# Kernel optimization log

Hardware: AMD Instinct MI355X
Metric: run time of the kernel (lower is better)

Reference implementation:

```python
import jax, jax.numpy as jnp
import numpy as np

N = 50000   # drug nodes
R = 8       # relations (= n_classes)
E = 200000  # edges per relation
ED = 400000 # decoder edges


def _deg_norm(idx, n):
    deg = jax.ops.segment_sum(jnp.ones(idx.shape, jnp.float32), idx, num_segments=n)
    return jnp.where(deg > 0, jax.lax.rsqrt(jnp.maximum(deg, 1.0)), 0.0)


def hetero_conv(x, src, dst, W, b, n):
    # DGL HeteroGraphConv(sum) of GraphConv(norm='both') per relation, single node type.
    out = jnp.zeros((n, W.shape[2]), x.dtype)
    for r in range(W.shape[0]):
        s, d = src[r], dst[r]
        ns = _deg_norm(s, n)  # out-degree^{-1/2} (src norm)
        nd = _deg_norm(d, n)  # in-degree^{-1/2} (dst norm)
        m = (x * ns[:, None]) @ W[r]                       # [n, dout]
        agg = jax.ops.segment_sum(m[s], d, num_segments=n)  # gather+scatter [E, dout]
        out = out + agg * nd[:, None] + b[r]
    return out


def hgcn_layer(x, src, dst, Wa, ba, Wb, bb, n):
    h = hetero_conv(x, src, dst, Wa, ba, n)
    h = jax.nn.relu(h)
    return hetero_conv(h, src, dst, Wb, bb, n)


def setup_inputs() -> dict:
    key = jax.random.key(0)
    ks = jax.random.split(key, 16)
    s = 0.02
    return {
        "node2_features": jax.random.normal(ks[0], (N, 256), jnp.float32),
        "mpnn_features": jax.random.normal(ks[1], (N, 300), jnp.float32),
        "src": jax.random.randint(ks[2], (R, E), 0, N, jnp.int32),
        "dst": jax.random.randint(ks[3], (R, E), 0, N, jnp.int32),
        "dec_src": jax.random.randint(ks[4], (ED,), 0, N, jnp.int32),
        "dec_dst": jax.random.randint(ks[5], (ED,), 0, N, jnp.int32),
        "W2a": jax.random.normal(ks[6], (R, 256, 256), jnp.float32) * s,
        "b2a": jnp.zeros((R, 256), jnp.float32),
        "W2b": jax.random.normal(ks[7], (R, 256, 128), jnp.float32) * s,
        "b2b": jnp.zeros((R, 128), jnp.float32),
        "W3a": jax.random.normal(ks[8], (R, 300, 256), jnp.float32) * s,
        "b3a": jnp.zeros((R, 256), jnp.float32),
        "W3b": jax.random.normal(ks[9], (R, 256, 128), jnp.float32) * s,
        "b3b": jnp.zeros((R, 128), jnp.float32),
        "Wp1": jax.random.normal(ks[10], (512, 256), jnp.float32) * s,
        "bp1": jnp.zeros((256,), jnp.float32),
        "Wp2": jax.random.normal(ks[11], (256, R), jnp.float32) * s,
        "bp2": jnp.zeros((R,), jnp.float32),
    }


def reference(node2_features, mpnn_features, src, dst, dec_src, dec_dst,
              W2a, b2a, W2b, b2b, W3a, b3a, W3b, b3b, Wp1, bp1, Wp2, bp2):
    h2 = hgcn_layer(node2_features, src, dst, W2a, b2a, W2b, b2b, N)  # [N, 128]
    h3 = hgcn_layer(mpnn_features, src, dst, W3a, b3a, W3b, b3b, N)   # [N, 128]
    feat = jnp.concatenate([h2, h3], axis=1)                            # [N, 256]
    # edge-wise gather-concat-MLP (note: original has NO relu between W1 and W2)
    x = jnp.concatenate([feat[dec_src], feat[dec_dst]], axis=1)          # [ED, 512]
    score = (x @ Wp1 + bp1) @ Wp2 + bp2                                  # [ED, R]
    return score
```

## Files before the change

kernel.cpp:

```cpp
#include <hip/hip_runtime.h>
#include <hip/hip_bf16.h>

#define NN 50000
#define RR 8
#define EE 200000
#define EDD 400000
#define SCB 196
#define CH 5000

typedef __attribute__((ext_vector_type(8))) short short8;
typedef __attribute__((ext_vector_type(4))) float floatx4;

static __device__ __forceinline__ unsigned short f2bf(float f) {
    union { float f; unsigned u; } v; v.f = f;
    unsigned r = v.u + 0x7fff + ((v.u >> 16) & 1);
    return (unsigned short)(r >> 16);
}
static __device__ __forceinline__ float bf2f(unsigned short h) {
    union { unsigned u; float f; } v; v.u = ((unsigned)h) << 16;
    return v.f;
}
static __device__ __forceinline__ void gload_lds16(const unsigned short* g, unsigned short* l) {
    __builtin_amdgcn_global_load_lds(
        (const __attribute__((address_space(1))) void*)g,
        (__attribute__((address_space(3))) void*)l,
        16, 0, 0);
}

__global__ void k_hist(const int* __restrict__ src, const int* __restrict__ dst,
                       int* __restrict__ outdeg, int* __restrict__ indeg) {
    int i = blockIdx.x * blockDim.x + threadIdx.x;
    if (i >= RR * EE) return;
    int r = i / EE;
    int base = r * NN;
    atomicAdd(&outdeg[base + src[i]], 1);
    atomicAdd(&indeg[base + dst[i]], 1);
}

__global__ void k_norms(int* __restrict__ outdeg, int* __restrict__ indeg) {
    int i = blockIdx.x * blockDim.x + threadIdx.x;
    if (i >= RR * NN) return;
    int od = outdeg[i];
    int id = indeg[i];
    ((float*)outdeg)[i] = od > 0 ? rsqrtf((float)od) : 0.f;
    ((float*)indeg)[i]  = id > 0 ? rsqrtf((float)id) : 0.f;
}

__global__ void k_scanA(const int* __restrict__ indeg, int* __restrict__ bsum) {
    int r = blockIdx.y;
    int i = blockIdx.x * 256 + threadIdx.x;
    int v = (i < NN) ? indeg[(size_t)r * NN + i] : 0;
    #pragma unroll
    for (int d = 32; d > 0; d >>= 1) v += __shfl_down(v, d, 64);
    __shared__ int ws4[4];
    if ((threadIdx.x & 63) == 0) ws4[threadIdx.x >> 6] = v;
    __syncthreads();
    if (threadIdx.x == 0) bsum[r * SCB + blockIdx.x] = ws4[0] + ws4[1] + ws4[2] + ws4[3];
}

__global__ void k_scanB(int* __restrict__ bsum, int* __restrict__ offs) {
    int r = blockIdx.x;
    int t = threadIdx.x;
    int v = (t < SCB) ? bsum[r * SCB + t] : 0;
    int lane = t & 63, wid = t >> 6;
    int sv = v;
    #pragma unroll
    for (int d = 1; d < 64; d <<= 1) {
        int u = __shfl_up(sv, d, 64);
        if (lane >= d) sv += u;
    }
    __shared__ int wsum[4];
    if (lane == 63) wsum[wid] = sv;
    __syncthreads();
    int add = 0;
    for (int x = 0; x < wid; x++) add += wsum[x];
    int incl = sv + add;
    if (t < SCB) bsum[r * SCB + t] = incl - v;
    if (t == 255) offs[(size_t)r * (NN + 1) + NN] = incl;
}

__global__ void k_scanC(const int* __restrict__ indeg, const int* __restrict__ bsum,
                        int* __restrict__ offs) {
    int r = blockIdx.y;
    int i = blockIdx.x * 256 + threadIdx.x;
    int v = (i < NN) ? indeg[(size_t)r * NN + i] : 0;
    int lane = threadIdx.x & 63, wid = threadIdx.x >> 6;
    int sv = v;
    #pragma unroll
    for (int d = 1; d < 64; d <<= 1) {
        int u = __shfl_up(sv, d, 64);
        if (lane >= d) sv += u;
    }
    __shared__ int wsum[4];
    if (lane == 63) wsum[wid] = sv;
    __syncthreads();
    int add = bsum[r * SCB + blockIdx.x];
    for (int x = 0; x < wid; x++) add += wsum[x];
    if (i < NN) offs[(size_t)r * (NN + 1) + i] = sv - v + add;
}

__global__ void k_fillw(const int* __restrict__ src, const int* __restrict__ dst,
                        const int* __restrict__ offs, const float* __restrict__ ns,
                        int* __restrict__ cursor, int2* __restrict__ csrw) {
    int i = blockIdx.x * blockDim.x + threadIdx.x;
    if (i >= RR * EE) return;
    int r = i / EE;
    int s = src[i], d = dst[i];
    int pos = offs[r * (NN + 1) + d] + atomicAdd(&cursor[r * NN + d], 1);
    int2 v;
    v.x = s;
    v.y = __float_as_int(ns[(size_t)r * NN + s]);
    csrw[(size_t)r * EE + pos] = v;
}

__global__ void k_prep(const float* __restrict__ Wp1, const float* __restrict__ Wp2,
                       const float* __restrict__ bp1, const float* __restrict__ bp2,
                       const float* __restrict__ b2a, const float* __restrict__ b2b,
                       const float* __restrict__ b3a, const float* __restrict__ b3b,
                       float* __restrict__ Mcat, float* __restrict__ cvec,
                       float* __restrict__ bs) {
    int bx = blockIdx.x;
    if (bx < 16) {
        int t = bx * 256 + threadIdx.x;
        int i = t >> 4, j = t & 15;
        int half = j >> 3, jj = j & 7;
        const float* wrow = Wp1 + (size_t)(half * 256 + i) * 256;
        float s = 0.f;
        for (int k = 0; k < 256; k++) s += wrow[k] * Wp2[k * 8 + jj];
        Mcat[i * 16 + j] = s;
    } else if (bx == 16) {
        int j = threadIdx.x;
        if (j < 8) {
            float s = bp2[j];
            for (int k = 0; k < 256; k++) s += bp1[k] * Wp2[k * 8 + j];
            cvec[j] = s;
        }
    } else {
        int j = threadIdx.x;
        float s = 0.f;
        for (int r = 0; r < RR; r++) s += b2a[r * 256 + j];
        bs[j] = s;
        if (j < 128) {
            s = 0.f;
            for (int r = 0; r < RR; r++) s += b2b[r * 128 + j];
            bs[256 + j] = s;
        }
        s = 0.f;
        for (int r = 0; r < RR; r++) s += b3a[r * 256 + j];
        bs[512 + j] = s;
        if (j < 128) {
            s = 0.f;
            for (int r = 0; r < RR; r++) s += b3b[r * 128 + j];
            bs[768 + j] = s;
        }
    }
}

__global__ void k_fold(const float* __restrict__ W2b, const float* __restrict__ W3b,
                       const float* __restrict__ Mcat, const float* __restrict__ bs,
                       unsigned short* __restrict__ FmatT, float* __restrict__ cfold) {
    int bx = blockIdx.x;
    if (bx < 256) {
        int idx = bx * 256 + threadIdx.x;
        int rj = idx >> 9, i = idx & 511;
        int r = rj >> 4, j = rj & 15;
        float s = 0.f;
        if (i < 256) {
            const float* wr = W2b + ((size_t)r * 256 + i) * 128;
            for (int c = 0; c < 128; c++) s += wr[c] * Mcat[c * 16 + j];
        } else {
            const float* wr = W3b + ((size_t)r * 256 + (i - 256)) * 128;
            for (int c = 0; c < 128; c++) s += wr[c] * Mcat[(128 + c) * 16 + j];
        }
        FmatT[(size_t)rj * 512 + i] = f2bf(s);
    } else {
        int j = threadIdx.x;
        if (j < 16) {
            float s = 0.f;
            for (int c = 0; c < 128; c++)
                s += bs[256 + c] * Mcat[c * 16 + j] + bs[768 + c] * Mcat[(128 + c) * 16 + j];
            cfold[j] = s;
        }
    }
}

__global__ void k_castx(const float* __restrict__ x2, const float* __restrict__ x3,
                        unsigned short* __restrict__ XH) {
    int i = blockIdx.x * 256 + threadIdx.x;
    if (i >= NN * 560) return;
    int row = i / 560, col = i - row * 560;
    float v;
    if (col < 256) v = x2[(size_t)row * 256 + col];
    else if (col < 556) v = x3[(size_t)row * 300 + (col - 256)];
    else v = 0.f;
    XH[i] = f2bf(v);
}

__global__ void k_wt2(const float* __restrict__ W2a, const float* __restrict__ W3a,
                      unsigned short* __restrict__ WT2, unsigned short* __restrict__ WT3) {
    const float* W; unsigned short* WT; int K0, Kpad;
    if (blockIdx.y == 0) { W = W2a; WT = WT2; K0 = 256; Kpad = 256; }
    else                 { W = W3a; WT = WT3; K0 = 300; Kpad = 304; }
    int i = blockIdx.x * 256 + threadIdx.x;
    int total = 256 * RR * Kpad;
    if (i >= total) return;
    int n = i / (RR * Kpad);
    int rem = i - n * (RR * Kpad);
    int r = rem / Kpad;
    int k = rem - r * Kpad;
    float v = (k < K0) ? W[((size_t)r * K0 + k) * 256 + n] : 0.f;
    WT[i] = f2bf(v);
}

__global__ __launch_bounds__(256) void k_aggp(
        const unsigned short* __restrict__ xb,
        const int2* __restrict__ csrw, const int* __restrict__ offs,
        const float* __restrict__ nd, int nbase,
        unsigned short* __restrict__ Y2, unsigned short* __restrict__ Y3) {
    int lane = threadIdx.x & 63;
    int sub = threadIdx.x >> 6;
    int bn = blockIdx.x * 4 + sub;
    int n = nbase + bn;
    int r = blockIdx.y;
    int o0 = offs[r * (NN + 1) + n];
    int o1 = offs[r * (NN + 1) + n + 1];
    o0 = __builtin_amdgcn_readfirstlane(o0);
    o1 = __builtin_amdgcn_readfirstlane(o1);
    float ndv = nd[(size_t)r * NN + n];
    const int2* cs = csrw + (size_t)r * EE;
    bool ex = lane < 12;
    float pa[4], qa[4], xa[4];
    #pragma unroll
    for (int q = 0; q < 4; q++) { pa[q] = 0.f; qa[q] = 0.f; xa[q] = 0.f; }
    int e = o0;
    for (; e + 4 <= o1; e += 4) {
        int2 w0 = cs[e], w1 = cs[e + 1], w2 = cs[e + 2], w3 = cs[e + 3];
        const unsigned short* p0 = xb + (size_t)(unsigned)w0.x * 560;
        const unsigned short* p1 = xb + (size_t)(unsigned)w1.x * 560;
        const unsigned short* p2 = xb + (size_t)(unsigned)w2.x * 560;
        const unsigned short* p3 = xb + (size_t)(unsigned)w3.x * 560;
        ushort4 a0 = *(const ushort4*)(p0 + lane * 4);
        ushort4 a1 = *(const ushort4*)(p1 + lane * 4);
        ushort4 a2 = *(const ushort4*)(p2 + lane * 4);
        ushort4 a3 = *(const ushort4*)(p3 + lane * 4);
        ushort4 b0 = *(const ushort4*)(p0 + 256 + lane * 4);
        ushort4 b1 = *(const ushort4*)(p1 + 256 + lane * 4);
        ushort4 b2 = *(const ushort4*)(p2 + 256 + lane * 4);
        ushort4 b3 = *(const ushort4*)(p3 + 256 + lane * 4);
        float f0 = __int_as_float(w0.y), f1 = __int_as_float(w1.y);
        float f2 = __int_as_float(w2.y), f3 = __int_as_float(w3.y);
        pa[0] += f0 * bf2f(a0.x) + f1 * bf2f(a1.x) + f2 * bf2f(a2.x) + f3 * bf2f(a3.x);
        pa[1] += f0 * bf2f(a0.y) + f1 * bf2f(a1.y) + f2 * bf2f(a2.y) + f3 * bf2f(a3.y);
        pa[2] += f0 * bf2f(a0.z) + f1 * bf2f(a1.z) + f2 * bf2f(a2.z) + f3 * bf2f(a3.z);
        pa[3] += f0 * bf2f(a0.w) + f1 * bf2f(a1.w) + f2 * bf2f(a2.w) + f3 * bf2f(a3.w);
        qa[0] += f0 * bf2f(b0.x) + f1 * bf2f(b1.x) + f2 * bf2f(b2.x) + f3 * bf2f(b3.x);
        qa[1] += f0 * bf2f(b0.y) + f1 * bf2f(b1.y) + f2 * bf2f(b2.y) + f3 * bf2f(b3.y);
        qa[2] += f0 * bf2f(b0.z) + f1 * bf2f(b1.z) + f2 * bf2f(b2.z) + f3 * bf2f(b3.z);
        qa[3] += f0 * bf2f(b0.w) + f1 * bf2f(b1.w) + f2 * bf2f(b2.w) + f3 * bf2f(b3.w);
        if (ex) {
            ushort4 c0 = *(const ushort4*)(p0 + 512 + lane * 4);
            ushort4 c1 = *(const ushort4*)(p1 + 512 + lane * 4);
            ushort4 c2 = *(const ushort4*)(p2 + 512 + lane * 4);
            ushort4 c3 = *(const ushort4*)(p3 + 512 + lane * 4);
            xa[0] += f0 * bf2f(c0.x) + f1 * bf2f(c1.x) + f2 * bf2f(c2.x) + f3 * bf2f(c3.x);
            xa[1] += f0 * bf2f(c0.y) + f1 * bf2f(c1.y) + f2 * bf2f(c2.y) + f3 * bf2f(c3.y);
            xa[2] += f0 * bf2f(c0.z) + f1 * bf2f(c1.z) + f2 * bf2f(c2.z) + f3 * bf2f(c3.z);
            xa[3] += f0 * bf2f(c0.w) + f1 * bf2f(c1.w) + f2 * bf2f(c2.w) + f3 * bf2f(c3.w);
        }
    }
    for (; e < o1; e++) {
        int2 w0 = cs[e];
        const unsigned short* p0 = xb + (size_t)(unsigned)w0.x * 560;
        ushort4 a0 = *(const ushort4*)(p0 + lane * 4);
        ushort4 b0 = *(const ushort4*)(p0 + 256 + lane * 4);
        float f0 = __int_as_float(w0.y);
        pa[0] += f0 * bf2f(a0.x); pa[1] += f0 * bf2f(a0.y);
        pa[2] += f0 * bf2f(a0.z); pa[3] += f0 * bf2f(a0.w);
        qa[0] += f0 * bf2f(b0.x); qa[1] += f0 * bf2f(b0.y);
        qa[2] += f0 * bf2f(b0.z); qa[3] += f0 * bf2f(b0.w);
        if (ex) {
            ushort4 c0 = *(const ushort4*)(p0 + 512 + lane * 4);
            xa[0] += f0 * bf2f(c0.x); xa[1] += f0 * bf2f(c0.y);
            xa[2] += f0 * bf2f(c0.z); xa[3] += f0 * bf2f(c0.w);
        }
    }
    ushort4 op, oq;
    op.x = f2bf(pa[0] * ndv); op.y = f2bf(pa[1] * ndv);
    op.z = f2bf(pa[2] * ndv); op.w = f2bf(pa[3] * ndv);
    oq.x = f2bf(qa[0] * ndv); oq.y = f2bf(qa[1] * ndv);
    oq.z = f2bf(qa[2] * ndv); oq.w = f2bf(qa[3] * ndv);
    *(ushort4*)(Y2 + (size_t)bn * 2048 + r * 256 + lane * 4) = op;
    *(ushort4*)(Y3 + (size_t)bn * 2432 + r * 304 + lane * 4) = oq;
    if (ex) {
        ushort4 ox;
        ox.x = f2bf(xa[0] * ndv); ox.y = f2bf(xa[1] * ndv);
        ox.z = f2bf(xa[2] * ndv); ox.w = f2bf(xa[3] * ndv);
        *(ushort4*)(Y3 + (size_t)bn * 2432 + r * 304 + 256 + lane * 4) = ox;
    }
}

template<int TN>
__global__ __launch_bounds__(256) void k_gemm_bf(
        const unsigned short* __restrict__ A, int lda,
        const unsigned short* __restrict__ BT, int ldb,
        const float* __restrict__ bias,
        const float* __restrict__ Cin, int ldcin,
        void* __restrict__ Cout, int ldc,
        int M, int K, int flags) {
    constexpr int BN = TN * 32;
    __shared__ unsigned short As[128 * 64];
    __shared__ unsigned short Bs[BN * 64];
    int m0 = blockIdx.x * 128;
    int n0 = blockIdx.y * BN;
    int t = threadIdx.x;
    int w = t >> 6, l = t & 63;
    int qm = (w >> 1) * 64, qn = (w & 1) * (TN * 16);
    int lr = l & 15, lg = l >> 4;
    int lrow = l >> 3;
    int lch  = (l & 7) ^ lrow;

    floatx4 acc[4][TN];
    #pragma unroll
    for (int a = 0; a < 4; a++)
        #pragma unroll
        for (int b = 0; b < TN; b++)
            acc[a][b] = (floatx4){0.f, 0.f, 0.f, 0.f};

    for (int k0 = 0; k0 < K; k0 += 64) {
        #pragma unroll
        for (int j = 0; j < 4; j++) {
            int seg = w * 4 + j;
            int gr = m0 + seg * 8 + lrow; if (gr > M - 1) gr = M - 1;
            gload_lds16(A + (size_t)gr * lda + k0 + lch * 8, &As[seg * 512]);
        }
        #pragma unroll
        for (int j = 0; j < TN; j++) {
            int seg = w * TN + j;
            int row = n0 + seg * 8 + lrow;
            gload_lds16(BT + (size_t)row * ldb + k0 + lch * 8, &Bs[seg * 512]);
        }
        __syncthreads();
        #pragma unroll
        for (int ks = 0; ks < 2; ks++) {
            int slot = ((ks * 4 + lg) ^ (lr & 7)) * 8;
            short8 af[4], bf[TN];
            #pragma unroll
            for (int i = 0; i < 4; i++)
                af[i] = *(const short8*)&As[(qm + i * 16 + lr) * 64 + slot];
            #pragma unroll
            for (int i = 0; i < TN; i++)
                bf[i] = *(const short8*)&Bs[(qn + i * 16 + lr) * 64 + slot];
            #pragma unroll
            for (int tm = 0; tm < 4; tm++)
                #pragma unroll
                for (int tn = 0; tn < TN; tn++)
                    acc[tm][tn] = __builtin_amdgcn_mfma_f32_16x16x32_bf16(
                        af[tm], bf[tn], acc[tm][tn], 0, 0, 0);
        }
        __syncthreads();
    }

    int addbias = flags & 1, accum = flags & 2, relu = flags & 4, outbf = flags & 8;
    #pragma unroll
    for (int tm = 0; tm < 4; tm++) {
        int rbase = m0 + qm + tm * 16 + lg * 4;
        #pragma unroll
        for (int reg = 0; reg < 4; reg++) {
            int row = rbase + reg;
            if (row >= M) continue;
            #pragma unroll
            for (int tn = 0; tn < TN; tn++) {
                int col = n0 + qn + tn * 16 + lr;
                float v = acc[tm][tn][reg];
                if (addbias) v += bias[col];
                if (accum) v += Cin[(size_t)row * ldcin + col];
                if (relu) v = fmaxf(v, 0.f);
                if (outbf) ((unsigned short*)Cout)[(size_t)row * ldc + col] = f2bf(v);
                else       ((float*)Cout)[(size_t)row * ldc + col] = v;
            }
        }
    }
}

__global__ __launch_bounds__(256) void k_gemm2(
        const unsigned short* __restrict__ Y2, const unsigned short* __restrict__ Y3,
        const unsigned short* __restrict__ WT2, const unsigned short* __restrict__ WT3,
        const float* __restrict__ bs, unsigned short* __restrict__ hb,
        int nbase, int M) {
    constexpr int TN = 2;
    __shared__ unsigned short As[128 * 64];
    __shared__ unsigned short Bs[64 * 64];
    int z = blockIdx.z;
    const unsigned short* A  = z ? Y3 : Y2;
    const unsigned short* BT = z ? WT3 : WT2;
    int lda = z ? 2432 : 2048;
    int K = lda;
    const float* bias = bs + z * 512;
    int m0 = blockIdx.x * 128;
    int n0 = blockIdx.y * 64;
    int t = threadIdx.x;
    int w = t >> 6, l = t & 63;
    int qm = (w >> 1) * 64, qn = (w & 1) * 32;
    int lr = l & 15, lg = l >> 4;
    int lrow = l >> 3;
    int lch  = (l & 7) ^ lrow;

    floatx4 acc[4][TN];
    #pragma unroll
    for (int a = 0; a < 4; a++)
        #pragma unroll
        for (int b = 0; b < TN; b++)
            acc[a][b] = (floatx4){0.f, 0.f, 0.f, 0.f};

    for (int k0 = 0; k0 < K; k0 += 64) {
        #pragma unroll
        for (int j = 0; j < 4; j++) {
            int seg = w * 4 + j;
            int gr = m0 + seg * 8 + lrow; if (gr > M - 1) gr = M - 1;
            gload_lds16(A + (size_t)gr * lda + k0 + lch * 8, &As[seg * 512]);
        }
        #pragma unroll
        for (int j = 0; j < TN; j++) {
            int seg = w * TN + j;
            int row = n0 + seg * 8 + lrow;
            gload_lds16(BT + (size_t)row * lda + k0 + lch * 8, &Bs[seg * 512]);
        }
        __syncthreads();
        #pragma unroll
        for (int ks = 0; ks < 2; ks++) {
            int slot = ((ks * 4 + lg) ^ (lr & 7)) * 8;
            short8 af[4], bf[TN];
            #pragma unroll
            for (int i = 0; i < 4; i++)
                af[i] = *(const short8*)&As[(qm + i * 16 + lr) * 64 + slot];
            #pragma unroll
            for (int i = 0; i < TN; i++)
                bf[i] = *(const short8*)&Bs[(qn + i * 16 + lr) * 64 + slot];
            #pragma unroll
            for (int tm = 0; tm < 4; tm++)
                #pragma unroll
                for (int tn = 0; tn < TN; tn++)
                    acc[tm][tn] = __builtin_amdgcn_mfma_f32_16x16x32_bf16(
                        af[tm], bf[tn], acc[tm][tn], 0, 0, 0);
        }
        __syncthreads();
    }

    #pragma unroll
    for (int tm = 0; tm < 4; tm++) {
        int rbase = m0 + qm + tm * 16 + lg * 4;
        #pragma unroll
        for (int reg = 0; reg < 4; reg++) {
            int row = rbase + reg;
            if (row >= M) continue;
            #pragma unroll
            for (int tn = 0; tn < TN; tn++) {
                int col = n0 + qn + tn * 16 + lr;
                float v = fmaxf(acc[tm][tn][reg] + bias[col], 0.f);
                hb[(size_t)(nbase + row) * 512 + z * 256 + col] = f2bf(v);
            }
        }
    }
}

__global__ __launch_bounds__(256) void k_aggAB(
        const int2* __restrict__ csrw, const int* __restrict__ offs,
        const float* __restrict__ nd, const float* __restrict__ G,
        const float* __restrict__ cfold, float* __restrict__ AB) {
    int lane = threadIdx.x & 63, sub = threadIdx.x >> 6;
    int n = blockIdx.x * 4 + sub;
    int slot = lane >> 4, j = lane & 15;
    float acc = 0.f;
    for (int r = 0; r < RR; r++) {
        int o0 = offs[r * (NN + 1) + n];
        int o1 = offs[r * (NN + 1) + n + 1];
        o0 = __builtin_amdgcn_readfirstlane(o0);
        o1 = __builtin_amdgcn_readfirstlane(o1);
        float ndv = nd[(size_t)r * NN + n];
        const int2* cs = csrw + (size_t)r * EE;
        float tr = 0.f;
        for (int e = o0 + slot; e < o1; e += 4) {
            int2 w = cs[e];
            tr += __int_as_float(w.y) * G[(size_t)(unsigned)w.x * 128 + r * 16 + j];
        }
        acc += ndv * tr;
    }
    acc += __shfl_xor(acc, 16, 64);
    acc += __shfl_xor(acc, 32, 64);
    if (lane < 16) AB[(size_t)n * 16 + j] = acc + cfold[j];
}

__global__ void k_dec(const int* __restrict__ dsrc, const int* __restrict__ ddst,
                      const float* __restrict__ AB, const float* __restrict__ cvec,
                      float* __restrict__ out) {
    int i = blockIdx.x * blockDim.x + threadIdx.x;
    if (i >= EDD * 8) return;
    int e = i >> 3, k = i & 7;
    out[i] = AB[dsrc[e] * 16 + k] + AB[ddst[e] * 16 + 8 + k] + cvec[k];
}

extern "C" void kernel_launch(void* const* d_in, const int* in_sizes, int n_in,
                              void* d_out, int out_size, void* d_ws, size_t ws_size,
                              hipStream_t stream) {
    const float* x2  = (const float*)d_in[0];
    const float* x3  = (const float*)d_in[1];
    const int*   src = (const int*)d_in[2];
    const int*   dst = (const int*)d_in[3];
    const int*   dsrc = (const int*)d_in[4];
    const int*   ddst = (const int*)d_in[5];
    const float* W2a = (const float*)d_in[6];
    const float* b2a = (const float*)d_in[7];
    const float* W2b = (const float*)d_in[8];
    const float* b2b = (const float*)d_in[9];
    const float* W3a = (const float*)d_in[10];
    const float* b3a = (const float*)d_in[11];
    const float* W3b = (const float*)d_in[12];
    const float* b3b = (const float*)d_in[13];
    const float* Wp1 = (const float*)d_in[14];
    const float* bp1 = (const float*)d_in[15];
    const float* Wp2 = (const float*)d_in[16];
    const float* bp2 = (const float*)d_in[17];
    float* out = (float*)d_out;

    char* ws = (char*)d_ws;
    size_t off = 0;
    auto alloc = [&](size_t nbytes) {
        char* p = ws + off;
        off += nbytes;
        off = (off + 255) & ~(size_t)255;
        return p;
    };
    float* ns   = (float*)alloc((size_t)RR * NN * 4);
    float* nd   = (float*)alloc((size_t)RR * NN * 4);
    int*   offs = (int*)alloc((size_t)RR * (NN + 1) * 4);
    int2*  csrw = (int2*)alloc((size_t)RR * EE * 8);
    unsigned short* XH     = (unsigned short*)alloc((size_t)NN * 560 * 2);
    unsigned short* hbuf23 = (unsigned short*)alloc((size_t)NN * 512 * 2);
    unsigned short* WT2a   = (unsigned short*)alloc((size_t)256 * 2048 * 2);
    unsigned short* WT3a   = (unsigned short*)alloc((size_t)256 * 2432 * 2);
    unsigned short* FmatT  = (unsigned short*)alloc((size_t)128 * 512 * 2);
    char* YR = alloc((size_t)CH * (2048 + 2432) * 2);
    float* Mcat  = (float*)alloc(4096 * 4);
    float* cvec  = (float*)alloc(64 * 4);
    float* bsums = (float*)alloc(1024 * 4);
    float* cfold = (float*)alloc(64 * 4);
    int*   bsum  = (int*)alloc((size_t)RR * SCB * 4);

    unsigned short* Y2a = (unsigned short*)YR;
    unsigned short* Y3a = Y2a + (size_t)CH * 2048;
    int*   outdeg = (int*)ns;
    int*   indeg  = (int*)nd;
    int*   cursor = (int*)YR;
    float* G      = (float*)YR;
    float* AB     = (float*)(YR + (size_t)NN * 128 * 4);

    hipMemsetAsync(outdeg, 0, (size_t)RR * NN * 4, stream);
    hipMemsetAsync(indeg,  0, (size_t)RR * NN * 4, stream);
    hipMemsetAsync(cursor, 0, (size_t)RR * NN * 4, stream);

    int edgeBlocks = (RR * EE + 255) / 256;
    k_hist<<<edgeBlocks, 256, 0, stream>>>(src, dst, outdeg, indeg);
    k_scanA<<<dim3(SCB, RR), 256, 0, stream>>>(indeg, bsum);
    k_scanB<<<RR, 256, 0, stream>>>(bsum, offs);
    k_scanC<<<dim3(SCB, RR), 256, 0, stream>>>(indeg, bsum, offs);
    k_norms<<<(RR * NN + 255) / 256, 256, 0, stream>>>(outdeg, indeg);
    k_fillw<<<edgeBlocks, 256, 0, stream>>>(src, dst, offs, ns, cursor, csrw);
    k_prep<<<18, 256, 0, stream>>>(Wp1, Wp2, bp1, bp2, b2a, b2b, b3a, b3b, Mcat, cvec, bsums);
    k_fold<<<257, 256, 0, stream>>>(W2b, W3b, Mcat, bsums, FmatT, cfold);

    k_castx<<<(NN * 560 + 255) / 256, 256, 0, stream>>>(x2, x3, XH);
    k_wt2<<<dim3((256 * RR * 304 + 255) / 256, 2), 256, 0, stream>>>(W2a, W3a, WT2a, WT3a);

    for (int c = 0; c < NN / CH; c++) {
        k_aggp<<<dim3(CH / 4, RR), 256, 0, stream>>>(XH, csrw, offs, nd, c * CH, Y2a, Y3a);
        k_gemm2<<<dim3((CH + 127) / 128, 4, 2), 256, 0, stream>>>(
            Y2a, Y3a, WT2a, WT3a, bsums, hbuf23, c * CH, CH);
    }

    k_gemm_bf<1><<<dim3((NN + 127) / 128, 4), 256, 0, stream>>>(
        hbuf23, 512, FmatT, 512, bsums, (const float*)nullptr, 0,
        (void*)G, 128, NN, 512, 0);

    k_aggAB<<<NN / 4, 256, 0, stream>>>(csrw, offs, nd, G, cfold, AB);
    k_dec<<<(EDD * 8 + 255) / 256, 256, 0, stream>>>(dsrc, ddst, AB, cvec, out);
}
```

Before: 1.261 ms.

## Use LDS-privatized degree histograms, 16-byte gathers in aggregation, and vectorized decoder

```diff
diff --git a/kernel.cpp b/kernel.cpp
--- a/kernel.cpp
+++ b/kernel.cpp
@@ -7,6 +7,7 @@
 #define EDD 400000
 #define SCB 196
 #define CH 5000
+#define CHK 16
 
 typedef __attribute__((ext_vector_type(8))) short short8;
 typedef __attribute__((ext_vector_type(4))) float floatx4;
@@ -27,14 +28,45 @@
         16, 0, 0);
 }
 
-__global__ void k_hist(const int* __restrict__ src, const int* __restrict__ dst,
-                       int* __restrict__ outdeg, int* __restrict__ indeg) {
-    int i = blockIdx.x * blockDim.x + threadIdx.x;
-    if (i >= RR * EE) return;
-    int r = i / EE;
-    int base = r * NN;
-    atomicAdd(&outdeg[base + src[i]], 1);
-    atomicAdd(&indeg[base + dst[i]], 1);
+__global__ __launch_bounds__(256) void k_histp(const int* __restrict__ src, const int* __restrict__ dst,
+                                               unsigned char* __restrict__ tmp) {
+    __shared__ unsigned lh[12512];
+    int chunk = blockIdx.x, r = blockIdx.y, which = blockIdx.z;
+    const int* idx = (which ? dst : src) + (size_t)r * EE;
+    for (int i = threadIdx.x; i < 12512; i += 256) lh[i] = 0;
+    __syncthreads();
+    int e0 = chunk * (EE / CHK);
+    for (int e = e0 + threadIdx.x; e < e0 + EE / CHK; e += 256) {
+        int n = idx[e];
+        atomicAdd(&lh[n >> 2], 1u << ((n & 3) * 8));
+    }
+    __syncthreads();
+    unsigned* t = (unsigned*)(tmp + (((size_t)(which * RR + r) * CHK + chunk) * 50048));
+    for (int i = threadIdx.x; i < 12512; i += 256) t[i] = lh[i];
+}
+
+__global__ void k_reduce(const unsigned char* __restrict__ tmp,
+                         int* __restrict__ outdeg, int* __restrict__ indeg) {
+    int i = blockIdx.x * 256 + threadIdx.x;
+    if (i >= 2 * RR * 12512) return;
+    int wr = i / 12512;
+    int wd = i - wr * 12512;
+    unsigned s0 = 0, s1 = 0, s2 = 0, s3 = 0;
+    const unsigned* base = (const unsigned*)(tmp + (size_t)wr * CHK * 50048) + wd;
+    #pragma unroll
+    for (int c = 0; c < CHK; c++) {
+        unsigned v = base[(size_t)c * 12512];
+        s0 += v & 255u; s1 += (v >> 8) & 255u; s2 += (v >> 16) & 255u; s3 += (v >> 24) & 255u;
+    }
+    int which = wr / RR, r = wr - which * RR;
+    int n = wd * 4;
+    int* deg = (which ? indeg : outdeg) + (size_t)r * NN;
+    if (n < NN) {
+        deg[n] = (int)s0;
+        if (n + 1 < NN) deg[n + 1] = (int)s1;
+        if (n + 2 < NN) deg[n + 2] = (int)s2;
+        if (n + 3 < NN) deg[n + 3] = (int)s3;
+    }
 }
 
 __global__ void k_norms(int* __restrict__ outdeg, int* __restrict__ indeg) {
@@ -219,6 +251,8 @@
         unsigned short* __restrict__ Y2, unsigned short* __restrict__ Y3) {
     int lane = threadIdx.x & 63;
     int sub = threadIdx.x >> 6;
+    int h = lane >> 5;
+    int l = lane & 31;
     int bn = blockIdx.x * 4 + sub;
     int n = nbase + bn;
     int r = blockIdx.y;
@@ -228,74 +262,71 @@
     o1 = __builtin_amdgcn_readfirstlane(o1);
     float ndv = nd[(size_t)r * NN + n];
     const int2* cs = csrw + (size_t)r * EE;
-    bool ex = lane < 12;
-    float pa[4], qa[4], xa[4];
-    #pragma unroll
-    for (int q = 0; q < 4; q++) { pa[q] = 0.f; qa[q] = 0.f; xa[q] = 0.f; }
+    bool tl = l < 6;
+    float va[8], vb[8], vc[8];
+    #pragma unroll
+    for (int q = 0; q < 8; q++) { va[q] = 0.f; vb[q] = 0.f; vc[q] = 0.f; }
     int e = o0;
-    for (; e + 4 <= o1; e += 4) {
-        int2 w0 = cs[e], w1 = cs[e + 1], w2 = cs[e + 2], w3 = cs[e + 3];
-        const unsigned short* p0 = xb + (size_t)(unsigned)w0.x * 560;
-        const unsigned short* p1 = xb + (size_t)(unsigned)w1.x * 560;
-        const unsigned short* p2 = xb + (size_t)(unsigned)w2.x * 560;
-        const unsigned short* p3 = xb + (size_t)(unsigned)w3.x * 560;
-        ushort4 a0 = *(const ushort4*)(p0 + lane * 4);
-        ushort4 a1 = *(const ushort4*)(p1 + lane * 4);
-        ushort4 a2 = *(const ushort4*)(p2 + lane * 4);
-        ushort4 a3 = *(const ushort4*)(p3 + lane * 4);
-        ushort4 b0 = *(const ushort4*)(p0 + 256 + lane * 4);
-        ushort4 b1 = *(const ushort4*)(p1 + 256 + lane * 4);
-        ushort4 b2 = *(const ushort4*)(p2 + 256 + lane * 4);
-        ushort4 b3 = *(const ushort4*)(p3 + 256 + lane * 4);
-        float f0 = __int_as_float(w0.y), f1 = __int_as_float(w1.y);
-        float f2 = __int_as_float(w2.y), f3 = __int_as_float(w3.y);
-        pa[0] += f0 * bf2f(a0.x) + f1 * bf2f(a1.x) + f2 * bf2f(a2.x) + f3 * bf2f(a3.x);
-        pa[1] += f0 * bf2f(a0.y) + f1 * bf2f(a1.y) + f2 * bf2f(a2.y) + f3 * bf2f(a3.y);
-        pa[2] += f0 * bf2f(a0.z) + f1 * bf2f(a1.z) + f2 * bf2f(a2.z) + f3 * bf2f(a3.z);
-        pa[3] += f0 * bf2f(a0.w) + f1 * bf2f(a1.w) + f2 * bf2f(a2.w) + f3 * bf2f(a3.w);
-        qa[0] += f0 * bf2f(b0.x) + f1 * bf2f(b1.x) + f2 * bf2f(b2.x) + f3 * bf2f(b3.x);
-        qa[1] += f0 * bf2f(b0.y) + f1 * bf2f(b1.y) + f2 * bf2f(b2.y) + f3 * bf2f(b3.y);
-        qa[2] += f0 * bf2f(b0.z) + f1 * bf2f(b1.z) + f2 * bf2f(b2.z) + f3 * bf2f(b3.z);
-        qa[3] += f0 * bf2f(b0.w) + f1 * bf2f(b1.w) + f2 * bf2f(b2.w) + f3 * bf2f(b3.w);
-        if (ex) {
-            ushort4 c0 = *(const ushort4*)(p0 + 512 + lane * 4);
-            ushort4 c1 = *(const ushort4*)(p1 + 512 + lane * 4);
-            ushort4 c2 = *(const ushort4*)(p2 + 512 + lane * 4);
-            ushort4 c3 = *(const ushort4*)(p3 + 512 + lane * 4);
-            xa[0] += f0 * bf2f(c0.x) + f1 * bf2f(c1.x) + f2 * bf2f(c2.x) + f3 * bf2f(c3.x);
-            xa[1] += f0 * bf2f(c0.y) + f1 * bf2f(c1.y) + f2 * bf2f(c2.y) + f3 * bf2f(c3.y);
-            xa[2] += f0 * bf2f(c0.z) + f1 * bf2f(c1.z) + f2 * bf2f(c2.z) + f3 * bf2f(c3.z);
-            xa[3] += f0 * bf2f(c0.w) + f1 * bf2f(c1.w) + f2 * bf2f(c2.w) + f3 * bf2f(c3.w);
-        }
-    }
-    for (; e < o1; e++) {
-        int2 w0 = cs[e];
-        const unsigned short* p0 = xb + (size_t)(unsigned)w0.x * 560;
-        ushort4 a0 = *(const ushort4*)(p0 + lane * 4);
-        ushort4 b0 = *(const ushort4*)(p0 + 256 + lane * 4);
-        float f0 = __int_as_float(w0.y);
-        pa[0] += f0 * bf2f(a0.x); pa[1] += f0 * bf2f(a0.y);
-        pa[2] += f0 * bf2f(a0.z); pa[3] += f0 * bf2f(a0.w);
-        qa[0] += f0 * bf2f(b0.x); qa[1] += f0 * bf2f(b0.y);
-        qa[2] += f0 * bf2f(b0.z); qa[3] += f0 * bf2f(b0.w);
-        if (ex) {
-            ushort4 c0 = *(const ushort4*)(p0 + 512 + lane * 4);
-            xa[0] += f0 * bf2f(c0.x); xa[1] += f0 * bf2f(c0.y);
-            xa[2] += f0 * bf2f(c0.z); xa[3] += f0 * bf2f(c0.w);
-        }
-    }
-    ushort4 op, oq;
-    op.x = f2bf(pa[0] * ndv); op.y = f2bf(pa[1] * ndv);
-    op.z = f2bf(pa[2] * ndv); op.w = f2bf(pa[3] * ndv);
-    oq.x = f2bf(qa[0] * ndv); oq.y = f2bf(qa[1] * ndv);
-    oq.z = f2bf(qa[2] * ndv); oq.w = f2bf(qa[3] * ndv);
-    *(ushort4*)(Y2 + (size_t)bn * 2048 + r * 256 + lane * 4) = op;
-    *(ushort4*)(Y3 + (size_t)bn * 2432 + r * 304 + lane * 4) = oq;
-    if (ex) {
-        ushort4 ox;
-        ox.x = f2bf(xa[0] * ndv); ox.y = f2bf(xa[1] * ndv);
-        ox.z = f2bf(xa[2] * ndv); ox.w = f2bf(xa[3] * ndv);
-        *(ushort4*)(Y3 + (size_t)bn * 2432 + r * 304 + 256 + lane * 4) = ox;
+    for (; e + 8 <= o1; e += 8) {
+        #pragma unroll
+        for (int u = 0; u < 4; u++) {
+            int2 w = cs[e + 2 * u + h];
+            const unsigned short* p = xb + (size_t)(unsigned)w.x * 560;
+            short8 A = *(const short8*)(p + l * 8);
+            short8 B = *(const short8*)(p + 256 + l * 8);
+            float f = __int_as_float(w.y);
+            #pragma unroll
+            for (int q = 0; q < 8; q++) {
+                va[q] += f * bf2f((unsigned short)A[q]);
+                vb[q] += f * bf2f((unsigned short)B[q]);
+            }
+            if (tl) {
+                short8 C = *(const short8*)(p + 512 + l * 8);
+                #pragma unroll
+                for (int q = 0; q < 8; q++) vc[q] += f * bf2f((unsigned short)C[q]);
+            }
+        }
+    }
+    for (; e < o1; e += 2) {
+        int ee = e + h;
+        bool valid = ee < o1;
+        int2 w = cs[valid ? ee : e];
+        float f = valid ? __int_as_float(w.y) : 0.f;
+        const unsigned short* p = xb + (size_t)(unsigned)w.x * 560;
+        short8 A = *(const short8*)(p + l * 8);
+        short8 B = *(const short8*)(p + 256 + l * 8);
+        #pragma unroll
+        for (int q = 0; q < 8; q++) {
+            va[q] += f * bf2f((unsigned short)A[q]);
+            vb[q] += f * bf2f((unsigned short)B[q]);
+        }
+        if (tl) {
+            short8 C = *(const short8*)(p + 512 + l * 8);
+            #pragma unroll
+            for (int q = 0; q < 8; q++) vc[q] += f * bf2f((unsigned short)C[q]);
+        }
+    }
+    #pragma unroll
+    for (int q = 0; q < 8; q++) {
+        va[q] += __shfl_xor(va[q], 32, 64);
+        vb[q] += __shfl_xor(vb[q], 32, 64);
+        vc[q] += __shfl_xor(vc[q], 32, 64);
+    }
+    if (h == 0) {
+        short8 o2, o3;
+        #pragma unroll
+        for (int q = 0; q < 8; q++) {
+            o2[q] = (short)f2bf(va[q] * ndv);
+            o3[q] = (short)f2bf(vb[q] * ndv);
+        }
+        *(short8*)(Y2 + (size_t)bn * 2048 + r * 256 + l * 8) = o2;
+        *(short8*)(Y3 + (size_t)bn * 2432 + r * 304 + l * 8) = o3;
+        if (tl) {
+            short8 oc;
+            #pragma unroll
+            for (int q = 0; q < 8; q++) oc[q] = (short)f2bf(vc[q] * ndv);
+            *(short8*)(Y3 + (size_t)bn * 2432 + r * 304 + 256 + l * 8) = oc;
+        }
     }
 }
 
@@ -466,7 +497,8 @@
 __global__ __launch_bounds__(256) void k_aggAB(
         const int2* __restrict__ csrw, const int* __restrict__ offs,
         const float* __restrict__ nd, const float* __restrict__ G,
-        const float* __restrict__ cfold, float* __restrict__ AB) {
+        const float* __restrict__ cfold, const float* __restrict__ cvec,
+        float* __restrict__ AB) {
     int lane = threadIdx.x & 63, sub = threadIdx.x >> 6;
     int n = blockIdx.x * 4 + sub;
     int slot = lane >> 4, j = lane & 15;
@@ -487,16 +519,21 @@
     }
     acc += __shfl_xor(acc, 16, 64);
     acc += __shfl_xor(acc, 32, 64);
-    if (lane < 16) AB[(size_t)n * 16 + j] = acc + cfold[j];
+    if (lane < 16) AB[(size_t)n * 16 + j] = acc + cfold[j] + (j < 8 ? cvec[j] : 0.f);
 }
 
 __global__ void k_dec(const int* __restrict__ dsrc, const int* __restrict__ ddst,
-                      const float* __restrict__ AB, const float* __restrict__ cvec,
-                      float* __restrict__ out) {
-    int i = blockIdx.x * blockDim.x + threadIdx.x;
-    if (i >= EDD * 8) return;
-    int e = i >> 3, k = i & 7;
-    out[i] = AB[dsrc[e] * 16 + k] + AB[ddst[e] * 16 + 8 + k] + cvec[k];
+                      const float* __restrict__ AB, float* __restrict__ out) {
+    int e = blockIdx.x * 256 + threadIdx.x;
+    if (e >= EDD) return;
+    int s = dsrc[e], d = ddst[e];
+    const float4* as = (const float4*)(AB + (size_t)s * 16);
+    const float4* ad = (const float4*)(AB + (size_t)d * 16 + 8);
+    float4 x0 = as[0], x1 = as[1], y0 = ad[0], y1 = ad[1];
+    float4 o0 = {x0.x + y0.x, x0.y + y0.y, x0.z + y0.z, x0.w + y0.w};
+    float4 o1 = {x1.x + y1.x, x1.y + y1.y, x1.z + y1.z, x1.w + y1.w};
+    float4* op = (float4*)(out + (size_t)e * 8);
+    op[0] = o0; op[1] = o1;
 }
 
 extern "C" void kernel_launch(void* const* d_in, const int* in_sizes, int n_in,
@@ -551,19 +588,19 @@
     int*   outdeg = (int*)ns;
     int*   indeg  = (int*)nd;
     int*   cursor = (int*)YR;
+    unsigned char* htmp = (unsigned char*)(YR + (4 << 20));
     float* G      = (float*)YR;
     float* AB     = (float*)(YR + (size_t)NN * 128 * 4);
 
-    hipMemsetAsync(outdeg, 0, (size_t)RR * NN * 4, stream);
-    hipMemsetAsync(indeg,  0, (size_t)RR * NN * 4, stream);
     hipMemsetAsync(cursor, 0, (size_t)RR * NN * 4, stream);
 
-    int edgeBlocks = (RR * EE + 255) / 256;
-    k_hist<<<edgeBlocks, 256, 0, stream>>>(src, dst, outdeg, indeg);
+    k_histp<<<dim3(CHK, RR, 2), 256, 0, stream>>>(src, dst, htmp);
+    k_reduce<<<(2 * RR * 12512 + 255) / 256, 256, 0, stream>>>(htmp, outdeg, indeg);
     k_scanA<<<dim3(SCB, RR), 256, 0, stream>>>(indeg, bsum);
     k_scanB<<<RR, 256, 0, stream>>>(bsum, offs);
     k_scanC<<<dim3(SCB, RR), 256, 0, stream>>>(indeg, bsum, offs);
     k_norms<<<(RR * NN + 255) / 256, 256, 0, stream>>>(outdeg, indeg);
+    int edgeBlocks = (RR * EE + 255) / 256;
     k_fillw<<<edgeBlocks, 256, 0, stream>>>(src, dst, offs, ns, cursor, csrw);
     k_prep<<<18, 256, 0, stream>>>(Wp1, Wp2, bp1, bp2, b2a, b2b, b3a, b3b, Mcat, cvec, bsums);
     k_fold<<<257, 256, 0, stream>>>(W2b, W3b, Mcat, bsums, FmatT, cfold);
@@ -581,6 +618,6 @@
         hbuf23, 512, FmatT, 512, bsums, (const float*)nullptr, 0,
         (void*)G, 128, NN, 512, 0);
 
-    k_aggAB<<<NN / 4, 256, 0, stream>>>(csrw, offs, nd, G, cfold, AB);
-    k_dec<<<(EDD * 8 + 255) / 256, 256, 0, stream>>>(dsrc, ddst, AB, cvec, out);
-}
+    k_aggAB<<<NN / 4, 256, 0, stream>>>(csrw, offs, nd, G, cfold, cvec, AB);
+    k_dec<<<(EDD + 255) / 256, 256, 0, stream>>>(dsrc, ddst, AB, out);
+}
```

New measurement: 1.195 ms. -5.2%, faster.
